# Optimization experiments

Hardware: AMD Instinct MI355X
Metric: run time of the kernel (lower is better)

Reference implementation:

```python
import jax, jax.numpy as jnp
import numpy as np

TOP_K = 2
BALANCE_COEFF = 0.01


def setup_inputs() -> dict:
    key = jax.random.key(0)
    ks = jax.random.split(key, 6)
    B, S, D, H, E = 2, 2048, 1024, 2048, 8
    return {
        "x": jax.random.normal(ks[0], (B, S, D), dtype=jnp.float32),
        "gate_w": jax.random.normal(ks[1], (E, D), dtype=jnp.float32) * 0.02,
        "w1": jax.random.normal(ks[2], (E, H, D), dtype=jnp.float32) * 0.02,
        "b1": jnp.zeros((E, H), dtype=jnp.float32),
        "w2": jax.random.normal(ks[3], (E, D, H), dtype=jnp.float32) * 0.02,
        "b2": jnp.zeros((E, D), dtype=jnp.float32),
    }


def reference(x, gate_w, w1, b1, w2, b2):
    B, S, D = x.shape
    E = gate_w.shape[0]
    xf = x.reshape(-1, D)                      # [N, D]
    N = xf.shape[0]

    # --- top-k gating (eval mode: no noise) ---
    logits = jnp.einsum("nd,ed->ne", xf, gate_w)          # [N, E]
    top_v, top_i = jax.lax.top_k(logits, TOP_K)           # [N, K]
    gates = jax.nn.softmax(top_v, axis=-1)                # [N, K]

    # load fraction per expert (no grad in original)
    counts = jnp.zeros((E,), dtype=xf.dtype).at[top_i.reshape(-1)].add(1.0)
    load = jax.lax.stop_gradient(counts / (N * TOP_K))    # [E]

    # combine weights: sum of gate weights routed to each expert per token
    comb = jnp.einsum("nk,nke->ne", gates, jax.nn.one_hot(top_i, E, dtype=gates.dtype))  # [N, E]

    # --- per-expert FFN (SiLU), weighted scatter-combine ---
    h = jax.nn.silu(jnp.einsum("nd,ehd->neh", xf, w1) + b1)   # [N, E, H]
    y = jnp.einsum("neh,edh->ned", h, w2) + b2                # [N, E, D]
    out = jnp.einsum("ned,ne->nd", y, comb).reshape(B, S, D)

    aux_loss = BALANCE_COEFF * E * jnp.sum(load * load)
    return out, aux_loss
```

## Files before the change

### kernel.cpp

```cpp
#include <hip/hip_runtime.h>
#include <stdint.h>

#define NTOK 4096
#define DDIM 1024
#define HDIM 2048
#define NEXP 8
#define TOPK 2

typedef short bf16x8 __attribute__((ext_vector_type(8)));
typedef float f32x4 __attribute__((ext_vector_type(4)));

__device__ __forceinline__ unsigned short f2bf(float f) {
    union { float f; unsigned int u; } v; v.f = f;
    unsigned int r = v.u + 0x7fffu + ((v.u >> 16) & 1u);
    return (unsigned short)(r >> 16);
}

__device__ __forceinline__ void gload16(const void* g, void* l) {
    __builtin_amdgcn_global_load_lds(
        (const __attribute__((address_space(1))) unsigned int*)g,
        (__attribute__((address_space(3))) unsigned int*)l, 16, 0, 0);
}

__global__ __launch_bounds__(256) void k_gate(
    const float* __restrict__ x, const float* __restrict__ gw,
    unsigned short* __restrict__ xb, int* __restrict__ cnt,
    int* __restrict__ topi, float* __restrict__ topg)
{
    int w = threadIdx.x >> 6, ln = threadIdx.x & 63;
    int n = blockIdx.x * 4 + w;
    const float* xr = x + (size_t)n * DDIM;
    float p[NEXP];
#pragma unroll
    for (int e = 0; e < NEXP; e++) p[e] = 0.f;
#pragma unroll
    for (int j = 0; j < DDIM / 64; j++) {
        int idx = ln + 64 * j;
        float xv = xr[idx];
        xb[(size_t)n * DDIM + idx] = f2bf(xv);
#pragma unroll
        for (int e = 0; e < NEXP; e++) p[e] += xv * gw[e * DDIM + idx];
    }
#pragma unroll
    for (int off = 32; off >= 1; off >>= 1) {
#pragma unroll
        for (int e = 0; e < NEXP; e++) p[e] += __shfl_xor(p[e], off, 64);
    }
    if (ln == 0) {
        int i0 = 0; float v0 = p[0];
#pragma unroll
        for (int e = 1; e < NEXP; e++) if (p[e] > v0) { v0 = p[e]; i0 = e; }
        int i1 = -1; float v1 = -3.0e38f;
#pragma unroll
        for (int e = 0; e < NEXP; e++) if (e != i0 && p[e] > v1) { v1 = p[e]; i1 = e; }
        float g0 = 1.f / (1.f + __expf(v1 - v0));
        float g1 = 1.f - g0;
        atomicAdd(&cnt[i0], 1); atomicAdd(&cnt[i1], 1);
        topi[n * 2] = i0; topi[n * 2 + 1] = i1;
        topg[n * 2] = g0; topg[n * 2 + 1] = g1;
    }
}

__global__ void k_scan(const int* __restrict__ cnt, int* __restrict__ offs,
                       float* __restrict__ auxout)
{
    if (threadIdx.x == 0) {
        int o = 0; float aux = 0.f;
#pragma unroll
        for (int e = 0; e < NEXP; e++) {
            offs[e] = o; o += cnt[e];
            float l = (float)cnt[e] / (float)(NTOK * TOPK);
            aux += l * l;
        }
        offs[NEXP] = o;
        auxout[0] = 0.01f * (float)NEXP * aux;
    }
}

__global__ __launch_bounds__(256) void k_scatter(
    const int* __restrict__ topi, const float* __restrict__ topg,
    const int* __restrict__ offs, int* __restrict__ fill,
    int* __restrict__ tok, float* __restrict__ gate)
{
    int g = blockIdx.x * 256 + threadIdx.x;
    if (g >= NTOK * TOPK) return;
    int e = topi[g];
    int pos = atomicAdd(&fill[e], 1);
    int slot = offs[e] + pos;
    tok[slot] = g >> 1;
    gate[slot] = topg[g];
}

__global__ __launch_bounds__(256) void k_conv(
    const float4* __restrict__ w1, const float4* __restrict__ w2,
    ushort4* __restrict__ w1b, ushort4* __restrict__ w2b)
{
    const int t1 = NEXP * HDIM * DDIM / 4;
    int stride = gridDim.x * blockDim.x;
    for (int i = blockIdx.x * 256 + threadIdx.x; i < 2 * t1; i += stride) {
        float4 v = (i < t1) ? w1[i] : w2[i - t1];
        ushort4 o;
        o.x = f2bf(v.x); o.y = f2bf(v.y); o.z = f2bf(v.z); o.w = f2bf(v.w);
        if (i < t1) w1b[i] = o; else w2b[i - t1] = o;
    }
}


#define VMCNT(n) asm volatile("s_waitcnt vmcnt(" #n ")" ::: "memory")
#define SBAR do { __builtin_amdgcn_sched_barrier(0); __builtin_amdgcn_s_barrier(); } while(0)
#define PRIO1 __builtin_amdgcn_s_setprio(1)
#define PRIO0 __builtin_amdgcn_s_setprio(0)

#define PH_STAGE_A(b,c,tt) gload16(aSrc[c] + (size_t)(tt)*64, smem + (b)*49152 + (c)*8192 + w*1024)
#define PH_STAGE_B(b,c,tt) do { \
    gload16(bSrc[c][0] + (size_t)(tt)*64, smem + (b)*49152 + 16384 + (c)*16384 + w*1024); \
    gload16(bSrc[c][1] + (size_t)(tt)*64, smem + (b)*49152 + 16384 + (c)*16384 + 8192 + w*1024); } while(0)

#define LDA_(b, mp) do { _Pragma("unroll") for (int mi=0;mi<2;mi++){ _Pragma("unroll") for(int k=0;k<2;k++){ \
    afr[mi][k] = *(const bf16x8*)(smem + (b)*49152 + (mp)*8192 + (wm*32 + mi*16 + ln15)*128 + colx[k]); }} } while(0)
#define LDB_(b, np, D) do { _Pragma("unroll") for (int ni=0;ni<2;ni++){ _Pragma("unroll") for(int k=0;k<2;k++){ \
    D[ni][k] = *(const bf16x8*)(smem + (b)*49152 + 16384 + (np)*16384 + (wn*32 + ni*16 + ln15)*128 + colx[k]); }} } while(0)
#define QUAD_(mp, np, D) do { _Pragma("unroll") for (int mi=0;mi<2;mi++){ _Pragma("unroll") for(int ni=0;ni<2;ni++){ _Pragma("unroll") for(int k=0;k<2;k++){ \
    acc[(mp)*2+mi][(np)*2+ni] = __builtin_amdgcn_mfma_f32_16x16x32_bf16(afr[mi][k], D[ni][k], acc[(mp)*2+mi][(np)*2+ni], 0,0,0); }}} } while(0)

#define ITER(LAST, t) do { \
   \
  LDA_(0,0); LDB_(0,0,bfa); PH_STAGE_A(1,1,(t)+1); \
  SBAR; PRIO1; QUAD_(0,0,bfa); PRIO0; SBAR; \
   \
  LDB_(0,1,bfb); if(!(LAST)) PH_STAGE_A(0,0,(t)+2); \
  SBAR; PRIO1; QUAD_(0,1,bfb); PRIO0; SBAR; \
   \
  LDA_(0,1); if(!(LAST)) PH_STAGE_B(0,0,(t)+2); \
  SBAR; PRIO1; QUAD_(1,1,bfb); PRIO0; SBAR; \
   \
  if(!(LAST)) PH_STAGE_B(0,1,(t)+2); \
  SBAR; PRIO1; QUAD_(1,0,bfa); PRIO0; \
  if(LAST) { VMCNT(0); } else { VMCNT(5); } SBAR; \
   \
  LDA_(1,0); LDB_(1,0,bfa); if(!(LAST)) PH_STAGE_A(0,1,(t)+2); \
  SBAR; PRIO1; QUAD_(0,0,bfa); PRIO0; SBAR; \
   \
  LDB_(1,1,bfb); if(!(LAST)) PH_STAGE_A(1,0,(t)+3); \
  SBAR; PRIO1; QUAD_(0,1,bfb); PRIO0; SBAR; \
   \
  LDA_(1,1); if(!(LAST)) PH_STAGE_B(1,0,(t)+3); \
  SBAR; PRIO1; QUAD_(1,1,bfb); PRIO0; SBAR; \
   \
  if(!(LAST)) PH_STAGE_B(1,1,(t)+3); \
  SBAR; PRIO1; QUAD_(1,0,bfa); PRIO0; \
  if(!(LAST)) { VMCNT(5); } SBAR; \
} while(0)

template<int KDIM, bool IS_FFN1>
__global__ __launch_bounds__(512, 2) void k_ffn8(
    const unsigned short* __restrict__ Abase,
    const unsigned short* __restrict__ Wb,
    const float* __restrict__ bias,
    const int* __restrict__ offs,
    const int* __restrict__ tok,
    const float* __restrict__ gate,
    unsigned short* __restrict__ hbuf,
    float* __restrict__ out)
{
    constexpr int NCOLS = IS_FFN1 ? HDIM : DDIM;
    constexpr int T = KDIM / 64;

    int e = blockIdx.y & 7, rt = blockIdx.y >> 3;
    int soff = offs[e];
    int n_e = offs[e + 1] - soff;
    int row0 = rt * 128;
    if (row0 >= n_e) return;
    int ncol0 = blockIdx.x * 256;

    __shared__ __align__(16) char smem[98304];

    int tid = threadIdx.x;
    int w = tid >> 6, ln = tid & 63;
    int wm = w >> 2, wn = w & 3;
    int ln15 = ln & 15, g4 = ln >> 4;
    int colx[2];
#pragma unroll
    for (int k = 0; k < 2; k++) colx[k] = ((g4 + k * 4) ^ (ln15 & 7)) * 16;

    const unsigned short* aSrc[2];
#pragma unroll
    for (int c = 0; c < 2; c++) {
        int rho = w * 8 + (ln >> 3);
        int trow = (rho >> 5) * 64 + c * 32 + (rho & 31);
        int csrc = (ln & 7) ^ ((ln >> 3) & 7);
        int r = row0 + trow; if (r > n_e - 1) r = n_e - 1;
        size_t grow = IS_FFN1 ? (size_t)tok[soff + r] : (size_t)(soff + r);
        aSrc[c] = Abase + grow * KDIM + csrc * 8;
    }
    const unsigned short* Wexp = Wb + (size_t)e * NCOLS * KDIM;
    const unsigned short* bSrc[2][2];
#pragma unroll
    for (int c = 0; c < 2; c++)
#pragma unroll
        for (int i = 0; i < 2; i++) {
            int lam = i * 512 + tid;
            int rho = lam >> 3;
            int tcol = (rho >> 5) * 64 + c * 32 + (rho & 31);
            int csrc = (tid & 7) ^ (rho & 7);
            bSrc[c][i] = Wexp + (size_t)(ncol0 + tcol) * KDIM + csrc * 8;
        }

    f32x4 acc[4][4];
#pragma unroll
    for (int m = 0; m < 4; m++)
#pragma unroll
        for (int n = 0; n < 4; n++) acc[m][n] = (f32x4)0.f;

    bf16x8 afr[2][2], bfa[2][2], bfb[2][2];

    PH_STAGE_A(0, 0, 0);
    PH_STAGE_B(0, 0, 0);
    PH_STAGE_B(0, 1, 0);
    PH_STAGE_A(0, 1, 0);
    PH_STAGE_A(1, 0, 1);
    PH_STAGE_B(1, 0, 1);
    PH_STAGE_B(1, 1, 1);
    VMCNT(5);
    SBAR;

    for (int t = 0; t + 2 < T; t += 2) ITER(false, t);
    ITER(true, T - 2);

    if (IS_FFN1) {
#pragma unroll
        for (int m = 0; m < 4; m++) {
#pragma unroll
            for (int q = 0; q < 4; q++) {
                int r = row0 + wm * 64 + m * 16 + g4 * 4 + q;
                if (r < n_e) {
#pragma unroll
                    for (int n = 0; n < 4; n++) {
                        int col = ncol0 + wn * 64 + n * 16 + ln15;
                        float v = acc[m][n][q] + bias[e * NCOLS + col];
                        float s = v / (1.f + __expf(-v));
                        hbuf[(size_t)(soff + r) * HDIM + col] = f2bf(s);
                    }
                }
            }
        }
    } else {
#pragma unroll
        for (int m = 0; m < 4; m++) {
#pragma unroll
            for (int q = 0; q < 4; q++) {
                int r = row0 + wm * 64 + m * 16 + g4 * 4 + q;
                if (r < n_e) {
                    int tk = tok[soff + r];
                    float gt = gate[soff + r];
#pragma unroll
                    for (int n = 0; n < 4; n++) {
                        int col = ncol0 + wn * 64 + n * 16 + ln15;
                        float v = gt * (acc[m][n][q] + bias[e * NCOLS + col]);
                        atomicAdd(&out[(size_t)tk * DDIM + col], v);
                    }
                }
            }
        }
    }
}

extern "C" void kernel_launch(void* const* d_in, const int* in_sizes, int n_in,
                              void* d_out, int out_size, void* d_ws, size_t ws_size,
                              hipStream_t stream)
{
    const float* x  = (const float*)d_in[0];
    const float* gw = (const float*)d_in[1];
    const float* w1 = (const float*)d_in[2];
    const float* b1 = (const float*)d_in[3];
    const float* w2 = (const float*)d_in[4];
    const float* b2 = (const float*)d_in[5];
    float* out = (float*)d_out;

    char* ws = (char*)d_ws;
    size_t off = 0;
    auto alloc = [&](size_t bytes) {
        char* p = ws + off; off += (bytes + 255) & ~(size_t)255; return p;
    };
    unsigned short* xb  = (unsigned short*)alloc((size_t)NTOK * DDIM * 2);
    unsigned short* w1b = (unsigned short*)alloc((size_t)NEXP * HDIM * DDIM * 2);
    unsigned short* w2b = (unsigned short*)alloc((size_t)NEXP * DDIM * HDIM * 2);
    unsigned short* hb  = (unsigned short*)alloc((size_t)NTOK * TOPK * HDIM * 2);
    int*   tok  = (int*)alloc(NTOK * TOPK * 4);
    float* gate = (float*)alloc(NTOK * TOPK * 4);
    int*   topi = (int*)alloc(NTOK * TOPK * 4);
    float* topg = (float*)alloc(NTOK * TOPK * 4);
    int*   ctrl = (int*)alloc(256);

    int* cnt  = ctrl;
    int* offs = ctrl + 16;
    int* fill = ctrl + 32;

    hipMemsetAsync(ctrl, 0, 256, stream);
    hipMemsetAsync(d_out, 0, (size_t)out_size * sizeof(float), stream);

    k_gate<<<NTOK / 4, 256, 0, stream>>>(x, gw, xb, cnt, topi, topg);
    k_scan<<<1, 64, 0, stream>>>(cnt, offs, out + (size_t)NTOK * DDIM);
    k_scatter<<<(NTOK * TOPK) / 256, 256, 0, stream>>>(topi, topg, offs, fill, tok, gate);
    k_conv<<<2048, 256, 0, stream>>>((const float4*)w1, (const float4*)w2,
                                     (ushort4*)w1b, (ushort4*)w2b);
    k_ffn8<DDIM, true ><<<dim3(HDIM / 256, (NTOK / 128) * NEXP), 512, 0, stream>>>(
        xb, w1b, b1, offs, tok, gate, hb, out);
    k_ffn8<HDIM, false><<<dim3(DDIM / 256, (NTOK / 128) * NEXP), 512, 0, stream>>>(
        hb, w2b, b2, offs, tok, gate, hb, out);
}
```

Baseline: 479.3 us.

## Enlarge expert GEMM row tile to 256 and split-K the second FFN

```diff
diff --git a/kernel.cpp b/kernel.cpp
--- a/kernel.cpp
+++ b/kernel.cpp
@@ -111,48 +111,50 @@
 #define PRIO1 __builtin_amdgcn_s_setprio(1)
 #define PRIO0 __builtin_amdgcn_s_setprio(0)
 
-#define PH_STAGE_A(b,c,tt) gload16(aSrc[c] + (size_t)(tt)*64, smem + (b)*49152 + (c)*8192 + w*1024)
-#define PH_STAGE_B(b,c,tt) do { \
-    gload16(bSrc[c][0] + (size_t)(tt)*64, smem + (b)*49152 + 16384 + (c)*16384 + w*1024); \
-    gload16(bSrc[c][1] + (size_t)(tt)*64, smem + (b)*49152 + 16384 + (c)*16384 + 8192 + w*1024); } while(0)
-
-#define LDA_(b, mp) do { _Pragma("unroll") for (int mi=0;mi<2;mi++){ _Pragma("unroll") for(int k=0;k<2;k++){ \
-    afr[mi][k] = *(const bf16x8*)(smem + (b)*49152 + (mp)*8192 + (wm*32 + mi*16 + ln15)*128 + colx[k]); }} } while(0)
-#define LDB_(b, np, D) do { _Pragma("unroll") for (int ni=0;ni<2;ni++){ _Pragma("unroll") for(int k=0;k<2;k++){ \
-    D[ni][k] = *(const bf16x8*)(smem + (b)*49152 + 16384 + (np)*16384 + (wn*32 + ni*16 + ln15)*128 + colx[k]); }} } while(0)
-#define QUAD_(mp, np, D) do { _Pragma("unroll") for (int mi=0;mi<2;mi++){ _Pragma("unroll") for(int ni=0;ni<2;ni++){ _Pragma("unroll") for(int k=0;k<2;k++){ \
-    acc[(mp)*2+mi][(np)*2+ni] = __builtin_amdgcn_mfma_f32_16x16x32_bf16(afr[mi][k], D[ni][k], acc[(mp)*2+mi][(np)*2+ni], 0,0,0); }}} } while(0)
+#define ST_A(b,h,tt) do { \
+    gload16(aSrc[h][0] + (size_t)(tt)*64, smem + (b)*65536 + (h)*16384 +        w*1024); \
+    gload16(aSrc[h][1] + (size_t)(tt)*64, smem + (b)*65536 + (h)*16384 + 8192 + w*1024); } while(0)
+#define ST_B(b,h,tt) do { \
+    gload16(bSrc[h][0] + (size_t)(tt)*64, smem + (b)*65536 + 32768 + (h)*16384 +        w*1024); \
+    gload16(bSrc[h][1] + (size_t)(tt)*64, smem + (b)*65536 + 32768 + (h)*16384 + 8192 + w*1024); } while(0)
+
+#define LDA(DST,b,mh) do { _Pragma("unroll") for (int mi=0;mi<4;mi++) { _Pragma("unroll") for (int ks=0;ks<2;ks++) { \
+    DST[mi][ks] = *(const bf16x8*)(smem + (b)*65536 + (mh)*16384 + (wm*64 + mi*16 + ln15)*128 + colx[ks]); }} } while(0)
+#define LDB(b,nh) do { _Pragma("unroll") for (int ni=0;ni<2;ni++) { _Pragma("unroll") for (int ks=0;ks<2;ks++) { \
+    bb[ni][ks] = *(const bf16x8*)(smem + (b)*65536 + 32768 + (nh)*16384 + (wn*32 + ni*16 + ln15)*128 + colx[ks]); }} } while(0)
+#define QUAD16(mh,nh,ASET) do { _Pragma("unroll") for (int mi=0;mi<4;mi++) { _Pragma("unroll") for (int ni=0;ni<2;ni++) { _Pragma("unroll") for (int ks=0;ks<2;ks++) { \
+    acc[(mh)*4+mi][(nh)*2+ni] = __builtin_amdgcn_mfma_f32_16x16x32_bf16(ASET[mi][ks], bb[ni][ks], acc[(mh)*4+mi][(nh)*2+ni], 0,0,0); }}} } while(0)
 
 #define ITER(LAST, t) do { \
    \
-  LDA_(0,0); LDB_(0,0,bfa); PH_STAGE_A(1,1,(t)+1); \
-  SBAR; PRIO1; QUAD_(0,0,bfa); PRIO0; SBAR; \
-   \
-  LDB_(0,1,bfb); if(!(LAST)) PH_STAGE_A(0,0,(t)+2); \
-  SBAR; PRIO1; QUAD_(0,1,bfb); PRIO0; SBAR; \
-   \
-  LDA_(0,1); if(!(LAST)) PH_STAGE_B(0,0,(t)+2); \
-  SBAR; PRIO1; QUAD_(1,1,bfb); PRIO0; SBAR; \
-   \
-  if(!(LAST)) PH_STAGE_B(0,1,(t)+2); \
-  SBAR; PRIO1; QUAD_(1,0,bfa); PRIO0; \
-  if(LAST) { VMCNT(0); } else { VMCNT(5); } SBAR; \
-   \
-  LDA_(1,0); LDB_(1,0,bfa); if(!(LAST)) PH_STAGE_A(0,1,(t)+2); \
-  SBAR; PRIO1; QUAD_(0,0,bfa); PRIO0; SBAR; \
-   \
-  LDB_(1,1,bfb); if(!(LAST)) PH_STAGE_A(1,0,(t)+3); \
-  SBAR; PRIO1; QUAD_(0,1,bfb); PRIO0; SBAR; \
-   \
-  LDA_(1,1); if(!(LAST)) PH_STAGE_B(1,0,(t)+3); \
-  SBAR; PRIO1; QUAD_(1,1,bfb); PRIO0; SBAR; \
-   \
-  if(!(LAST)) PH_STAGE_B(1,1,(t)+3); \
-  SBAR; PRIO1; QUAD_(1,0,bfa); PRIO0; \
-  if(!(LAST)) { VMCNT(5); } SBAR; \
+  LDA(aA,0,0); LDB(0,0); ST_A(1,1,(t)+1); \
+  SBAR; PRIO1; QUAD16(0,0,aA); PRIO0; SBAR; \
+   \
+  LDA(aB,0,1); if(!(LAST)) ST_A(0,0,(t)+2); \
+  SBAR; PRIO1; QUAD16(1,0,aB); PRIO0; SBAR; \
+   \
+  LDB(0,1); if(!(LAST)) ST_B(0,0,(t)+2); \
+  SBAR; PRIO1; QUAD16(1,1,aB); PRIO0; SBAR; \
+   \
+  if(!(LAST)) ST_B(0,1,(t)+2); \
+  SBAR; PRIO1; QUAD16(0,1,aA); PRIO0; \
+  if(LAST) { VMCNT(0); } else { VMCNT(6); } SBAR; \
+   \
+  LDA(aA,1,0); LDB(1,0); if(!(LAST)) ST_A(0,1,(t)+2); \
+  SBAR; PRIO1; QUAD16(0,0,aA); PRIO0; SBAR; \
+   \
+  LDA(aB,1,1); if(!(LAST)) ST_A(1,0,(t)+3); \
+  SBAR; PRIO1; QUAD16(1,0,aB); PRIO0; SBAR; \
+   \
+  LDB(1,1); if(!(LAST)) ST_B(1,0,(t)+3); \
+  SBAR; PRIO1; QUAD16(1,1,aB); PRIO0; SBAR; \
+   \
+  if(!(LAST)) ST_B(1,1,(t)+3); \
+  SBAR; PRIO1; QUAD16(0,1,aA); PRIO0; \
+  if(!(LAST)) { VMCNT(6); } SBAR; \
 } while(0)
 
-template<int KDIM, bool IS_FFN1>
+template<int KTOT, int TBLK, bool IS_FFN1>
 __global__ __launch_bounds__(512, 2) void k_ffn8(
     const unsigned short* __restrict__ Abase,
     const unsigned short* __restrict__ Wb,
@@ -164,16 +166,16 @@
     float* __restrict__ out)
 {
     constexpr int NCOLS = IS_FFN1 ? HDIM : DDIM;
-    constexpr int T = KDIM / 64;
 
     int e = blockIdx.y & 7, rt = blockIdx.y >> 3;
     int soff = offs[e];
     int n_e = offs[e + 1] - soff;
-    int row0 = rt * 128;
+    int row0 = rt * 256;
     if (row0 >= n_e) return;
     int ncol0 = blockIdx.x * 256;
-
-    __shared__ __align__(16) char smem[98304];
+    int koff = blockIdx.z * (TBLK * 64);
+
+    __shared__ __align__(16) char smem[131072];
 
     int tid = threadIdx.x;
     int w = tid >> 6, ln = tid & 63;
@@ -181,63 +183,68 @@
     int ln15 = ln & 15, g4 = ln >> 4;
     int colx[2];
 #pragma unroll
-    for (int k = 0; k < 2; k++) colx[k] = ((g4 + k * 4) ^ (ln15 & 7)) * 16;
-
-    const unsigned short* aSrc[2];
-#pragma unroll
-    for (int c = 0; c < 2; c++) {
-        int rho = w * 8 + (ln >> 3);
-        int trow = (rho >> 5) * 64 + c * 32 + (rho & 31);
-        int csrc = (ln & 7) ^ ((ln >> 3) & 7);
-        int r = row0 + trow; if (r > n_e - 1) r = n_e - 1;
-        size_t grow = IS_FFN1 ? (size_t)tok[soff + r] : (size_t)(soff + r);
-        aSrc[c] = Abase + grow * KDIM + csrc * 8;
-    }
-    const unsigned short* Wexp = Wb + (size_t)e * NCOLS * KDIM;
+    for (int ks = 0; ks < 2; ks++) colx[ks] = ((ks * 4 + g4) ^ (ln15 & 7)) * 16;
+
+    const unsigned short* aSrc[2][2];
+#pragma unroll
+    for (int h = 0; h < 2; h++)
+#pragma unroll
+        for (int i = 0; i < 2; i++) {
+            int rho = i * 64 + (tid >> 3);
+            int trow = (rho >> 6) * 128 + h * 64 + (rho & 63);
+            int csrc = (tid & 7) ^ (rho & 7);
+            int r = row0 + trow; if (r > n_e - 1) r = n_e - 1;
+            size_t grow = IS_FFN1 ? (size_t)tok[soff + r] : (size_t)(soff + r);
+            aSrc[h][i] = Abase + grow * KTOT + koff + csrc * 8;
+        }
+    const unsigned short* Wexp = Wb + (size_t)e * NCOLS * KTOT;
     const unsigned short* bSrc[2][2];
 #pragma unroll
-    for (int c = 0; c < 2; c++)
+    for (int h = 0; h < 2; h++)
 #pragma unroll
         for (int i = 0; i < 2; i++) {
-            int lam = i * 512 + tid;
-            int rho = lam >> 3;
-            int tcol = (rho >> 5) * 64 + c * 32 + (rho & 31);
+            int rho = i * 64 + (tid >> 3);
+            int tcol = (rho >> 5) * 64 + h * 32 + (rho & 31);
             int csrc = (tid & 7) ^ (rho & 7);
-            bSrc[c][i] = Wexp + (size_t)(ncol0 + tcol) * KDIM + csrc * 8;
-        }
-
-    f32x4 acc[4][4];
-#pragma unroll
-    for (int m = 0; m < 4; m++)
+            bSrc[h][i] = Wexp + (size_t)(ncol0 + tcol) * KTOT + koff + csrc * 8;
+        }
+
+    f32x4 acc[8][4];
+#pragma unroll
+    for (int m = 0; m < 8; m++)
 #pragma unroll
         for (int n = 0; n < 4; n++) acc[m][n] = (f32x4)0.f;
 
-    bf16x8 afr[2][2], bfa[2][2], bfb[2][2];
-
-    PH_STAGE_A(0, 0, 0);
-    PH_STAGE_B(0, 0, 0);
-    PH_STAGE_B(0, 1, 0);
-    PH_STAGE_A(0, 1, 0);
-    PH_STAGE_A(1, 0, 1);
-    PH_STAGE_B(1, 0, 1);
-    PH_STAGE_B(1, 1, 1);
-    VMCNT(5);
+    bf16x8 aA[4][2], aB[4][2], bb[2][2];
+
+    ST_A(0, 0, 0);
+    ST_B(0, 0, 0);
+    ST_A(0, 1, 0);
+    ST_B(0, 1, 0);
+    ST_A(1, 0, 1);
+    ST_B(1, 0, 1);
+    ST_B(1, 1, 1);
+    VMCNT(6);
     SBAR;
 
-    for (int t = 0; t + 2 < T; t += 2) ITER(false, t);
-    ITER(true, T - 2);
+    for (int t = 0; t + 2 < TBLK; t += 2) ITER(false, t);
+    ITER(true, TBLK - 2);
 
     if (IS_FFN1) {
-#pragma unroll
-        for (int m = 0; m < 4; m++) {
+        float bv[4];
+#pragma unroll
+        for (int nj = 0; nj < 4; nj++)
+            bv[nj] = bias[e * NCOLS + ncol0 + wn * 64 + nj * 16 + ln15];
+#pragma unroll
+        for (int mi = 0; mi < 8; mi++) {
 #pragma unroll
             for (int q = 0; q < 4; q++) {
-                int r = row0 + wm * 64 + m * 16 + g4 * 4 + q;
+                int r = row0 + wm * 128 + mi * 16 + g4 * 4 + q;
                 if (r < n_e) {
 #pragma unroll
-                    for (int n = 0; n < 4; n++) {
-                        int col = ncol0 + wn * 64 + n * 16 + ln15;
-                        float v = acc[m][n][q] + bias[e * NCOLS + col];
+                    for (int nj = 0; nj < 4; nj++) {
+                        int col = ncol0 + wn * 64 + nj * 16 + ln15;
+                        float v = acc[mi][nj][q] + bv[nj];
                         float s = v / (1.f + __expf(-v));
                         hbuf[(size_t)(soff + r) * HDIM + col] = f2bf(s);
                     }
@@ -245,18 +252,22 @@
             }
         }
     } else {
-#pragma unroll
-        for (int m = 0; m < 4; m++) {
+        float bv[4];
+#pragma unroll
+        for (int nj = 0; nj < 4; nj++)
+            bv[nj] = (koff == 0) ? bias[e * NCOLS + ncol0 + wn * 64 + nj * 16 + ln15] : 0.f;
+#pragma unroll
+        for (int mi = 0; mi < 8; mi++) {
 #pragma unroll
             for (int q = 0; q < 4; q++) {
-                int r = row0 + wm * 64 + m * 16 + g4 * 4 + q;
+                int r = row0 + wm * 128 + mi * 16 + g4 * 4 + q;
                 if (r < n_e) {
                     int tk = tok[soff + r];
                     float gt = gate[soff + r];
 #pragma unroll
-                    for (int n = 0; n < 4; n++) {
-                        int col = ncol0 + wn * 64 + n * 16 + ln15;
-                        float v = gt * (acc[m][n][q] + bias[e * NCOLS + col]);
+                    for (int nj = 0; nj < 4; nj++) {
+                        int col = ncol0 + wn * 64 + nj * 16 + ln15;
+                        float v = gt * (acc[mi][nj][q] + bv[nj]);
                         atomicAdd(&out[(size_t)tk * DDIM + col], v);
                     }
                 }
@@ -304,8 +315,8 @@
     k_scatter<<<(NTOK * TOPK) / 256, 256, 0, stream>>>(topi, topg, offs, fill, tok, gate);
     k_conv<<<2048, 256, 0, stream>>>((const float4*)w1, (const float4*)w2,
                                      (ushort4*)w1b, (ushort4*)w2b);
-    k_ffn8<DDIM, true ><<<dim3(HDIM / 256, (NTOK / 128) * NEXP), 512, 0, stream>>>(
+    k_ffn8<DDIM, 16, true ><<<dim3(HDIM / 256, 128, 1), 512, 0, stream>>>(
         xb, w1b, b1, offs, tok, gate, hb, out);
-    k_ffn8<HDIM, false><<<dim3(DDIM / 256, (NTOK / 128) * NEXP), 512, 0, stream>>>(
+    k_ffn8<HDIM, 16, false><<<dim3(DDIM / 256, 128, 2), 512, 0, stream>>>(
         hb, w2b, b2, offs, tok, gate, hb, out);
 }
```

New measurement: 540.9 us. +12.8%, slower.
